# Kernel tuning notes

Hardware: AMD Instinct MI355X
Metric: run time of the kernel (lower is better)

The kernel has to match this reference:

```python
import jax, jax.numpy as jnp
import numpy as np

DIM = 1024
NUM_HEADS = 16
HEAD_DIM = DIM // NUM_HEADS
SCALE = HEAD_DIM ** -0.5


def setup_inputs() -> dict:
    key = jax.random.key(0)
    ks = jax.random.split(key, 5)
    x = jax.random.normal(ks[0], (8, 1024, DIM), dtype=jnp.float32)
    # nn.Linear default init ~ U(-1/sqrt(fan_in), 1/sqrt(fan_in)); use scaled normals
    w_qkv = jax.random.normal(ks[1], (DIM, 3 * DIM), dtype=jnp.float32) * (DIM ** -0.5)
    b_qkv = jax.random.normal(ks[2], (3 * DIM,), dtype=jnp.float32) * 0.02
    w_proj = jax.random.normal(ks[3], (DIM, DIM), dtype=jnp.float32) * (DIM ** -0.5)
    b_proj = jax.random.normal(ks[4], (DIM,), dtype=jnp.float32) * 0.02
    return {"x": x, "w_qkv": w_qkv, "b_qkv": b_qkv, "w_proj": w_proj, "b_proj": b_proj}


def reference(x, w_qkv, b_qkv, w_proj, b_proj):
    B, N, D = x.shape
    qkv = x @ w_qkv + b_qkv                       # [B, N, 3D]
    qkv = qkv.reshape(B, N, 3, NUM_HEADS, HEAD_DIM)
    qkv = jnp.transpose(qkv, (2, 0, 3, 1, 4))     # [3, B, H, N, hd]
    q, k, v = qkv[0], qkv[1], qkv[2]
    attn = jnp.einsum('bhqd,bhkd->bhqk', q, k) * SCALE
    attn = jax.nn.softmax(attn, axis=-1)
    out = jnp.einsum('bhqk,bhkd->bhqd', attn, v)  # [B, H, N, hd]
    out = jnp.transpose(out, (0, 2, 1, 3)).reshape(B, N, D)
    out = out @ w_proj + b_proj
    return out
```

## Files before the change

kernel.cpp:

```cpp
#include <hip/hip_runtime.h>
#include <stdint.h>


typedef short bf16x8 __attribute__((ext_vector_type(8)));
typedef float f32x4 __attribute__((ext_vector_type(4)));

__device__ __forceinline__ short f32_bf16(float f) {
  uint32_t u = __builtin_bit_cast(uint32_t, f);
  u += 0x7FFFu + ((u >> 16) & 1u);
  return (short)(u >> 16);
}

__device__ __forceinline__ float bf16_f32(short s) {
  uint32_t u = ((uint32_t)(uint16_t)s) << 16;
  return __builtin_bit_cast(float, u);
}

__device__ __forceinline__ void gload_lds16(const void* g, void* l) {
  __builtin_amdgcn_global_load_lds(
      (const __attribute__((address_space(1))) uint32_t*)g,
      (__attribute__((address_space(3))) uint32_t*)l, 16, 0, 0);
}

__global__ __launch_bounds__(256) void convert_x_kernel(
    const float* __restrict__ x, short* __restrict__ xb) {
  int i = blockIdx.x * 256 + threadIdx.x;
  const float4 f0 = ((const float4*)x)[i * 2];
  const float4 f1 = ((const float4*)x)[i * 2 + 1];
  bf16x8 o;
  o[0] = f32_bf16(f0.x); o[1] = f32_bf16(f0.y);
  o[2] = f32_bf16(f0.z); o[3] = f32_bf16(f0.w);
  o[4] = f32_bf16(f1.x); o[5] = f32_bf16(f1.y);
  o[6] = f32_bf16(f1.z); o[7] = f32_bf16(f1.w);
  ((bf16x8*)xb)[i] = o;
}

__global__ __launch_bounds__(256) void transpose_w_kernel(
    const float* __restrict__ w, short* __restrict__ wt, int N) {
  __shared__ float tile[64][65];
  const int n0 = blockIdx.x * 64, k0 = blockIdx.y * 64;
  const int tr = threadIdx.x >> 6, tc = threadIdx.x & 63;
#pragma unroll
  for (int i = 0; i < 16; ++i) {
    int k = tr + i * 4;
    tile[k][tc] = w[(size_t)(k0 + k) * N + n0 + tc];
  }
  __syncthreads();
#pragma unroll
  for (int i = 0; i < 16; ++i) {
    int a = tr + i * 4;
    wt[(size_t)(n0 + a) * 1024 + k0 + tc] = f32_bf16(tile[tc][a]);
  }
}

__global__ __launch_bounds__(256, 2) void gemm_qkv_kernel(
    const short* __restrict__ A, const short* __restrict__ Bt,
    const float* __restrict__ bias, short* __restrict__ Qb,
    short* __restrict__ Kb, short* __restrict__ Vt) {
  __shared__ short Asm[128 * 64];
  __shared__ short Bsm[128 * 64];
  const int tid = threadIdx.x;
  const int lane = tid & 63;
  const int w = tid >> 6;
  const int wr = w >> 1, wc = w & 1;
  const int c = lane & 15, g = lane >> 4;

  const int NT = 24;
  const int tm = blockIdx.x / NT, tn = blockIdx.x % NT;
  const int m0 = tm * 128, n0 = tn * 128;

  f32x4 acc[4][4] = {};

  for (int k0 = 0; k0 < 1024; k0 += 64) {
#pragma unroll
    for (int i = 0; i < 4; ++i) {
      int ch = (w * 4 + i) * 64 + lane;
      int r = ch >> 3, c8 = ch & 7;
      gload_lds16(A + (size_t)(m0 + r) * 1024 + k0 + c8 * 8, &Asm[ch * 8]);
      gload_lds16(Bt + (size_t)(n0 + r) * 1024 + k0 + c8 * 8, &Bsm[ch * 8]);
    }
    asm volatile("s_waitcnt vmcnt(0)" ::: "memory");
    __syncthreads();
#pragma unroll
    for (int kk = 0; kk < 2; ++kk) {
      bf16x8 a[4], b[4];
#pragma unroll
      for (int m = 0; m < 4; ++m)
        a[m] = *(const bf16x8*)&Asm[(wr * 64 + m * 16 + c) * 64 + kk * 32 + 8 * g];
#pragma unroll
      for (int n = 0; n < 4; ++n)
        b[n] = *(const bf16x8*)&Bsm[(wc * 64 + n * 16 + c) * 64 + kk * 32 + 8 * g];
#pragma unroll
      for (int m = 0; m < 4; ++m)
#pragma unroll
        for (int n = 0; n < 4; ++n)
          acc[m][n] = __builtin_amdgcn_mfma_f32_16x16x32_bf16(a[m], b[n], acc[m][n], 0, 0, 0);
    }
    __syncthreads();
  }

#pragma unroll
  for (int m = 0; m < 4; ++m) {
    const int i_base = m0 + wr * 64 + m * 16 + 4 * g;
#pragma unroll
    for (int n = 0; n < 4; ++n) {
      const int j = n0 + wc * 64 + n * 16 + c;
      const float bj = bias[j];
      const int three = j >> 10, rem = j & 1023, h = rem >> 6, d = rem & 63;
#pragma unroll
      for (int r = 0; r < 4; ++r) {
        const int i = i_base + r;
        const int bb = i >> 10, nn = i & 1023;
        const int bh = bb * 16 + h;
        const short bv = f32_bf16(acc[m][n][r] + bj);
        if (three == 0)
          Qb[(size_t)(bh * 1024 + nn) * 64 + d] = bv;
        else if (three == 1)
          Kb[(size_t)(bh * 1024 + nn) * 64 + d] = bv;
        else
          Vt[(size_t)(bh * 64 + d) * 1024 + nn] = bv;
      }
    }
  }
}

__global__ __launch_bounds__(256, 2) void attn_kernel(
    const short* __restrict__ Qb, const short* __restrict__ Kb,
    const short* __restrict__ Vt, short* __restrict__ Ao) {
  __shared__ short Kf[8 * 64 * 8];
  __shared__ short Vf[8 * 64 * 8];
  __shared__ short Pl[4][16 * 72];

  const int tid = threadIdx.x, lane = tid & 63, w = tid >> 6;
  const int c = lane & 15, g = lane >> 4;
  const int bh = blockIdx.x >> 3, qb = blockIdx.x & 7;
  const int bb = bh >> 4, h = bh & 15;
  const int q0 = qb * 128 + w * 32;

  bf16x8 qf[2][2];
#pragma unroll
  for (int m = 0; m < 2; ++m)
#pragma unroll
    for (int ks = 0; ks < 2; ++ks)
      qf[m][ks] = *(const bf16x8*)(Qb + (size_t)(bh * 1024 + q0 + m * 16 + c) * 64 + ks * 32 + 8 * g);

  f32x4 o[2][4] = {};
  float mrun[2][4], lrun[2][4];
#pragma unroll
  for (int m = 0; m < 2; ++m)
#pragma unroll
    for (int r = 0; r < 4; ++r) { mrun[m][r] = -1e30f; lrun[m][r] = 0.f; }

  const int row_r = tid >> 2;
  const int seg = tid & 3;

  for (int t = 0; t < 16; ++t) {
    const int kv0 = t * 64;
    {
      const short* src = Kb + (size_t)(bh * 1024 + kv0 + row_r) * 64 + seg * 16;
      bf16x8 v0 = *(const bf16x8*)(src);
      bf16x8 v1 = *(const bf16x8*)(src + 8);
      const int kt = row_r >> 4;
#pragma unroll
      for (int hh = 0; hh < 2; ++hh) {
        const int d0 = seg * 16 + hh * 8;
        const int ks = d0 >> 5;
        const int slot = (row_r & 15) + 16 * ((d0 & 31) >> 3);
        *(bf16x8*)&Kf[((kt * 2 + ks) * 64 + slot) * 8] = hh ? v1 : v0;
      }
      const short* vsrc = Vt + (size_t)(bh * 64 + row_r) * 1024 + kv0 + seg * 16;
      bf16x8 u0 = *(const bf16x8*)(vsrc);
      bf16x8 u1 = *(const bf16x8*)(vsrc + 8);
      const int dt = row_r >> 4;
#pragma unroll
      for (int hh = 0; hh < 2; ++hh) {
        const int k0l = seg * 16 + hh * 8;
        const int kk = k0l >> 5;
        const int slot = (row_r & 15) + 16 * ((k0l & 31) >> 3);
        *(bf16x8*)&Vf[((dt * 2 + kk) * 64 + slot) * 8] = hh ? u1 : u0;
      }
    }
    __syncthreads();

#pragma unroll
    for (int m = 0; m < 2; ++m) {
      f32x4 s[4];
#pragma unroll
      for (int kt = 0; kt < 4; ++kt) {
        f32x4 sa = {};
#pragma unroll
        for (int ks = 0; ks < 2; ++ks) {
          bf16x8 kb = *(const bf16x8*)&Kf[((kt * 2 + ks) * 64 + lane) * 8];
          sa = __builtin_amdgcn_mfma_f32_16x16x32_bf16(qf[m][ks], kb, sa, 0, 0, 0);
        }
        s[kt] = sa;
      }
#pragma unroll
      for (int kt = 0; kt < 4; ++kt)
#pragma unroll
        for (int r = 0; r < 4; ++r) s[kt][r] *= 0.125f;

      float tmax[4], alpha[4], rsum[4];
#pragma unroll
      for (int r = 0; r < 4; ++r) {
        float v = fmaxf(fmaxf(s[0][r], s[1][r]), fmaxf(s[2][r], s[3][r]));
#pragma unroll
        for (int msk = 1; msk < 16; msk <<= 1) v = fmaxf(v, __shfl_xor(v, msk));
        float mnew = fmaxf(mrun[m][r], v);
        alpha[r] = __expf(mrun[m][r] - mnew);
        mrun[m][r] = mnew;
        rsum[r] = 0.f;
      }
#pragma unroll
      for (int dt = 0; dt < 4; ++dt)
#pragma unroll
        for (int r = 0; r < 4; ++r) o[m][dt][r] *= alpha[r];

#pragma unroll
      for (int kt = 0; kt < 4; ++kt)
#pragma unroll
        for (int r = 0; r < 4; ++r) {
          float p = __expf(s[kt][r] - mrun[m][r]);
          rsum[r] += p;
          Pl[w][(4 * g + r) * 72 + kt * 16 + c] = f32_bf16(p);
        }
#pragma unroll
      for (int r = 0; r < 4; ++r) {
        float v = rsum[r];
#pragma unroll
        for (int msk = 1; msk < 16; msk <<= 1) v += __shfl_xor(v, msk);
        lrun[m][r] = lrun[m][r] * alpha[r] + v;
      }

#pragma unroll
      for (int kk = 0; kk < 2; ++kk) {
        bf16x8 pa = *(const bf16x8*)&Pl[w][c * 72 + kk * 32 + 8 * g];
#pragma unroll
        for (int dt = 0; dt < 4; ++dt) {
          bf16x8 vb = *(const bf16x8*)&Vf[((dt * 2 + kk) * 64 + lane) * 8];
          o[m][dt] = __builtin_amdgcn_mfma_f32_16x16x32_bf16(pa, vb, o[m][dt], 0, 0, 0);
        }
      }
    }
    __syncthreads();
  }

#pragma unroll
  for (int m = 0; m < 2; ++m)
#pragma unroll
    for (int dt = 0; dt < 4; ++dt)
#pragma unroll
      for (int r = 0; r < 4; ++r) {
        const int n = q0 + m * 16 + 4 * g + r;
        const float v = o[m][dt][r] / lrun[m][r];
        Ao[(size_t)(bb * 1024 + n) * 1024 + h * 64 + dt * 16 + c] = f32_bf16(v);
      }
}

__global__ __launch_bounds__(256, 2) void gemm_proj_kernel(
    const short* __restrict__ A, const short* __restrict__ Bt,
    const float* __restrict__ bias, float* __restrict__ out) {
  __shared__ short Asm[128 * 64];
  __shared__ short Bsm[128 * 64];
  const int tid = threadIdx.x;
  const int lane = tid & 63;
  const int w = tid >> 6;
  const int wr = w >> 1, wc = w & 1;
  const int c = lane & 15, g = lane >> 4;

  const int NT = 8;
  const int tm = blockIdx.x / NT, tn = blockIdx.x % NT;
  const int m0 = tm * 128, n0 = tn * 128;

  f32x4 acc[4][4] = {};

  for (int k0 = 0; k0 < 1024; k0 += 64) {
#pragma unroll
    for (int i = 0; i < 4; ++i) {
      int ch = (w * 4 + i) * 64 + lane;
      int r = ch >> 3, c8 = ch & 7;
      gload_lds16(A + (size_t)(m0 + r) * 1024 + k0 + c8 * 8, &Asm[ch * 8]);
      gload_lds16(Bt + (size_t)(n0 + r) * 1024 + k0 + c8 * 8, &Bsm[ch * 8]);
    }
    asm volatile("s_waitcnt vmcnt(0)" ::: "memory");
    __syncthreads();
#pragma unroll
    for (int kk = 0; kk < 2; ++kk) {
      bf16x8 a[4], b[4];
#pragma unroll
      for (int m = 0; m < 4; ++m)
        a[m] = *(const bf16x8*)&Asm[(wr * 64 + m * 16 + c) * 64 + kk * 32 + 8 * g];
#pragma unroll
      for (int n = 0; n < 4; ++n)
        b[n] = *(const bf16x8*)&Bsm[(wc * 64 + n * 16 + c) * 64 + kk * 32 + 8 * g];
#pragma unroll
      for (int m = 0; m < 4; ++m)
#pragma unroll
        for (int n = 0; n < 4; ++n)
          acc[m][n] = __builtin_amdgcn_mfma_f32_16x16x32_bf16(a[m], b[n], acc[m][n], 0, 0, 0);
    }
    __syncthreads();
  }

#pragma unroll
  for (int m = 0; m < 4; ++m) {
    const int i_base = m0 + wr * 64 + m * 16 + 4 * g;
#pragma unroll
    for (int n = 0; n < 4; ++n) {
      const int j = n0 + wc * 64 + n * 16 + c;
      const float bj = bias[j];
#pragma unroll
      for (int r = 0; r < 4; ++r)
        out[(size_t)(i_base + r) * 1024 + j] = acc[m][n][r] + bj;
    }
  }
}

extern "C" void kernel_launch(void* const* d_in, const int* in_sizes, int n_in,
                              void* d_out, int out_size, void* d_ws, size_t ws_size,
                              hipStream_t stream) {
  const float* x = (const float*)d_in[0];
  const float* w_qkv = (const float*)d_in[1];
  const float* b_qkv = (const float*)d_in[2];
  const float* w_proj = (const float*)d_in[3];
  const float* b_proj = (const float*)d_in[4];
  float* out = (float*)d_out;

  char* ws = (char*)d_ws;
  const size_t XB_OFF = 0;
  const size_t WQKVT_OFF = 16777216;
  const size_t WPROJT_OFF = WQKVT_OFF + 6291456;
  const size_t Q_OFF = WPROJT_OFF + 2097152;
  const size_t K_OFF = Q_OFF + 16777216;
  const size_t VT_OFF = K_OFF + 16777216;
  short* xb = (short*)(ws + XB_OFF);
  short* wqkvT = (short*)(ws + WQKVT_OFF);
  short* wprojT = (short*)(ws + WPROJT_OFF);
  short* Qb = (short*)(ws + Q_OFF);
  short* Kb = (short*)(ws + K_OFF);
  short* Vt = (short*)(ws + VT_OFF);
  short* attn_o = xb;

  convert_x_kernel<<<dim3(4096), dim3(256), 0, stream>>>(x, xb);
  transpose_w_kernel<<<dim3(48, 16), dim3(256), 0, stream>>>(w_qkv, wqkvT, 3072);
  transpose_w_kernel<<<dim3(16, 16), dim3(256), 0, stream>>>(w_proj, wprojT, 1024);
  gemm_qkv_kernel<<<dim3(64 * 24), dim3(256), 0, stream>>>(xb, wqkvT, b_qkv, Qb, Kb, Vt);
  attn_kernel<<<dim3(1024), dim3(256), 0, stream>>>(Qb, Kb, Vt, attn_o);
  gemm_proj_kernel<<<dim3(64 * 8), dim3(256), 0, stream>>>(attn_o, wprojT, b_proj, out);
}
```

Measured before the change: 325.0 us.

## Restructure attention softmax with exp2, lazy rescale, transposed MFMA and register prefetch

```diff
diff --git a/kernel.cpp b/kernel.cpp
--- a/kernel.cpp
+++ b/kernel.cpp
@@ -4,6 +4,7 @@
 
 typedef short bf16x8 __attribute__((ext_vector_type(8)));
 typedef float f32x4 __attribute__((ext_vector_type(4)));
+typedef uint32_t u32x2 __attribute__((ext_vector_type(2)));
 
 __device__ __forceinline__ short f32_bf16(float f) {
   uint32_t u = __builtin_bit_cast(uint32_t, f);
@@ -11,9 +12,14 @@
   return (short)(u >> 16);
 }
 
-__device__ __forceinline__ float bf16_f32(short s) {
-  uint32_t u = ((uint32_t)(uint16_t)s) << 16;
-  return __builtin_bit_cast(float, u);
+__device__ __forceinline__ float exp2_fast(float x) {
+  float r; asm("v_exp_f32 %0, %1" : "=v"(r) : "v"(x)); return r;
+}
+
+__device__ __forceinline__ uint32_t cvt_pk_bf16(float lo, float hi) {
+  uint32_t r;
+  asm("v_cvt_pk_bf16_f32 %0, %1, %2" : "=v"(r) : "v"(lo), "v"(hi));
+  return r;
 }
 
 __device__ __forceinline__ void gload_lds16(const void* g, void* l) {
@@ -107,12 +113,13 @@
       const int j = n0 + wc * 64 + n * 16 + c;
       const float bj = bias[j];
       const int three = j >> 10, rem = j & 1023, h = rem >> 6, d = rem & 63;
+      const float sc = (three == 1) ? 0.18033688f : 1.0f;
 #pragma unroll
       for (int r = 0; r < 4; ++r) {
         const int i = i_base + r;
         const int bb = i >> 10, nn = i & 1023;
         const int bh = bb * 16 + h;
-        const short bv = f32_bf16(acc[m][n][r] + bj);
+        const short bv = f32_bf16((acc[m][n][r] + bj) * sc);
         if (three == 0)
           Qb[(size_t)(bh * 1024 + nn) * 64 + d] = bv;
         else if (three == 1)
@@ -127,9 +134,10 @@
 __global__ __launch_bounds__(256, 2) void attn_kernel(
     const short* __restrict__ Qb, const short* __restrict__ Kb,
     const short* __restrict__ Vt, short* __restrict__ Ao) {
-  __shared__ short Kf[8 * 64 * 8];
-  __shared__ short Vf[8 * 64 * 8];
-  __shared__ short Pl[4][16 * 72];
+  __shared__ __align__(16) char smem[25600];
+  short* Kf = (short*)smem;
+  short* Vf = (short*)(smem + 8192);
+  short* Pl = (short*)(smem + 16384);
 
   const int tid = threadIdx.x, lane = tid & 63, w = tid >> 6;
   const int c = lane & 15, g = lane >> 4;
@@ -145,43 +153,27 @@
       qf[m][ks] = *(const bf16x8*)(Qb + (size_t)(bh * 1024 + q0 + m * 16 + c) * 64 + ks * 32 + 8 * g);
 
   f32x4 o[2][4] = {};
-  float mrun[2][4], lrun[2][4];
-#pragma unroll
-  for (int m = 0; m < 2; ++m)
-#pragma unroll
-    for (int r = 0; r < 4; ++r) { mrun[m][r] = -1e30f; lrun[m][r] = 0.f; }
-
-  const int row_r = tid >> 2;
-  const int seg = tid & 3;
-
-  for (int t = 0; t < 16; ++t) {
-    const int kv0 = t * 64;
-    {
-      const short* src = Kb + (size_t)(bh * 1024 + kv0 + row_r) * 64 + seg * 16;
-      bf16x8 v0 = *(const bf16x8*)(src);
-      bf16x8 v1 = *(const bf16x8*)(src + 8);
-      const int kt = row_r >> 4;
-#pragma unroll
-      for (int hh = 0; hh < 2; ++hh) {
-        const int d0 = seg * 16 + hh * 8;
-        const int ks = d0 >> 5;
-        const int slot = (row_r & 15) + 16 * ((d0 & 31) >> 3);
-        *(bf16x8*)&Kf[((kt * 2 + ks) * 64 + slot) * 8] = hh ? v1 : v0;
-      }
-      const short* vsrc = Vt + (size_t)(bh * 64 + row_r) * 1024 + kv0 + seg * 16;
-      bf16x8 u0 = *(const bf16x8*)(vsrc);
-      bf16x8 u1 = *(const bf16x8*)(vsrc + 8);
-      const int dt = row_r >> 4;
-#pragma unroll
-      for (int hh = 0; hh < 2; ++hh) {
-        const int k0l = seg * 16 + hh * 8;
-        const int kk = k0l >> 5;
-        const int slot = (row_r & 15) + 16 * ((k0l & 31) >> 3);
-        *(bf16x8*)&Vf[((dt * 2 + kk) * 64 + slot) * 8] = hh ? u1 : u0;
-      }
-    }
-    __syncthreads();
-
+  float mrun[2] = {-3.0e38f, -3.0e38f};
+  float lrun[2] = {0.f, 0.f};
+
+  const int row_r = tid >> 2, seg = tid & 3;
+  const short* kp = Kb + (size_t)(bh * 1024 + row_r) * 64 + seg * 16;
+  const short* vp = Vt + (size_t)(bh * 64 + row_r) * 1024 + seg * 16;
+  short *kdst0, *kdst1, *vdst0, *vdst1;
+  {
+    const int d0a = seg * 16, d0b = seg * 16 + 8;
+    const int pa = (row_r >> 4) * 2 + (d0a >> 5);
+    const int pb = (row_r >> 4) * 2 + (d0b >> 5);
+    const int sa = (row_r & 15) + 16 * ((d0a & 31) >> 3);
+    const int sb = (row_r & 15) + 16 * ((d0b & 31) >> 3);
+    kdst0 = &Kf[(pa * 64 + sa) * 8]; kdst1 = &Kf[(pb * 64 + sb) * 8];
+    vdst0 = &Vf[(pa * 64 + sa) * 8]; vdst1 = &Vf[(pb * 64 + sb) * 8];
+  }
+
+  uint32_t* plw = (uint32_t*)(Pl + w * 1152);
+  const short* plr = Pl + w * 1152;
+
+  auto compute = [&]() {
 #pragma unroll
     for (int m = 0; m < 2; ++m) {
       f32x4 s[4];
@@ -191,70 +183,106 @@
 #pragma unroll
         for (int ks = 0; ks < 2; ++ks) {
           bf16x8 kb = *(const bf16x8*)&Kf[((kt * 2 + ks) * 64 + lane) * 8];
-          sa = __builtin_amdgcn_mfma_f32_16x16x32_bf16(qf[m][ks], kb, sa, 0, 0, 0);
+          sa = __builtin_amdgcn_mfma_f32_16x16x32_bf16(kb, qf[m][ks], sa, 0, 0, 0);
         }
         s[kt] = sa;
       }
+      float vmax = s[0][0];
 #pragma unroll
       for (int kt = 0; kt < 4; ++kt)
 #pragma unroll
-        for (int r = 0; r < 4; ++r) s[kt][r] *= 0.125f;
-
-      float tmax[4], alpha[4], rsum[4];
-#pragma unroll
-      for (int r = 0; r < 4; ++r) {
-        float v = fmaxf(fmaxf(s[0][r], s[1][r]), fmaxf(s[2][r], s[3][r]));
-#pragma unroll
-        for (int msk = 1; msk < 16; msk <<= 1) v = fmaxf(v, __shfl_xor(v, msk));
-        float mnew = fmaxf(mrun[m][r], v);
-        alpha[r] = __expf(mrun[m][r] - mnew);
-        mrun[m][r] = mnew;
-        rsum[r] = 0.f;
-      }
-#pragma unroll
-      for (int dt = 0; dt < 4; ++dt)
-#pragma unroll
-        for (int r = 0; r < 4; ++r) o[m][dt][r] *= alpha[r];
-
-#pragma unroll
-      for (int kt = 0; kt < 4; ++kt)
-#pragma unroll
-        for (int r = 0; r < 4; ++r) {
-          float p = __expf(s[kt][r] - mrun[m][r]);
-          rsum[r] += p;
-          Pl[w][(4 * g + r) * 72 + kt * 16 + c] = f32_bf16(p);
-        }
-#pragma unroll
-      for (int r = 0; r < 4; ++r) {
-        float v = rsum[r];
-#pragma unroll
-        for (int msk = 1; msk < 16; msk <<= 1) v += __shfl_xor(v, msk);
-        lrun[m][r] = lrun[m][r] * alpha[r] + v;
-      }
-
+        for (int r = 0; r < 4; ++r) vmax = fmaxf(vmax, s[kt][r]);
+      vmax = fmaxf(vmax, __shfl_xor(vmax, 16));
+      vmax = fmaxf(vmax, __shfl_xor(vmax, 32));
+      if (!__all(vmax <= mrun[m] + 8.0f)) {
+        float mnew = fmaxf(mrun[m], vmax);
+        float al = exp2_fast(mrun[m] - mnew);
+        lrun[m] *= al;
+#pragma unroll
+        for (int dt = 0; dt < 4; ++dt) o[m][dt] *= al;
+        mrun[m] = mnew;
+      }
+      float rs = 0.f;
+#pragma unroll
+      for (int kt = 0; kt < 4; ++kt) {
+        float p0 = exp2_fast(s[kt][0] - mrun[m]);
+        float p1 = exp2_fast(s[kt][1] - mrun[m]);
+        float p2 = exp2_fast(s[kt][2] - mrun[m]);
+        float p3 = exp2_fast(s[kt][3] - mrun[m]);
+        rs += (p0 + p1) + (p2 + p3);
+        u32x2 pk;
+        pk[0] = cvt_pk_bf16(p0, p1);
+        pk[1] = cvt_pk_bf16(p2, p3);
+        *(u32x2*)&plw[c * 36 + kt * 8 + 2 * g] = pk;
+      }
+      rs += __shfl_xor(rs, 16);
+      rs += __shfl_xor(rs, 32);
+      lrun[m] += rs;
 #pragma unroll
       for (int kk = 0; kk < 2; ++kk) {
-        bf16x8 pa = *(const bf16x8*)&Pl[w][c * 72 + kk * 32 + 8 * g];
+        bf16x8 pb = *(const bf16x8*)(plr + c * 72 + kk * 32 + 8 * g);
 #pragma unroll
         for (int dt = 0; dt < 4; ++dt) {
           bf16x8 vb = *(const bf16x8*)&Vf[((dt * 2 + kk) * 64 + lane) * 8];
-          o[m][dt] = __builtin_amdgcn_mfma_f32_16x16x32_bf16(pa, vb, o[m][dt], 0, 0, 0);
+          o[m][dt] = __builtin_amdgcn_mfma_f32_16x16x32_bf16(vb, pb, o[m][dt], 0, 0, 0);
         }
       }
     }
-    __syncthreads();
-  }
-
-#pragma unroll
-  for (int m = 0; m < 2; ++m)
+  };
+
+  bf16x8 ka0, ka1, va0, va1, kc0, kc1, vc0, vc1;
+  ka0 = *(const bf16x8*)(kp);     ka1 = *(const bf16x8*)(kp + 8);
+  va0 = *(const bf16x8*)(vp);     va1 = *(const bf16x8*)(vp + 8);
+
+  for (int t = 0; t < 16; t += 2) {
+    __syncthreads();
+    *(bf16x8*)kdst0 = ka0; *(bf16x8*)kdst1 = ka1;
+    *(bf16x8*)vdst0 = va0; *(bf16x8*)vdst1 = va1;
+    {
+      const short* kpt = kp + (size_t)(t + 1) * 4096;
+      const short* vpt = vp + (t + 1) * 64;
+      kc0 = *(const bf16x8*)(kpt); kc1 = *(const bf16x8*)(kpt + 8);
+      vc0 = *(const bf16x8*)(vpt); vc1 = *(const bf16x8*)(vpt + 8);
+    }
+    __syncthreads();
+    compute();
+    __syncthreads();
+    *(bf16x8*)kdst0 = kc0; *(bf16x8*)kdst1 = kc1;
+    *(bf16x8*)vdst0 = vc0; *(bf16x8*)vdst1 = vc1;
+    if (t + 2 < 16) {
+      const short* kpt = kp + (size_t)(t + 2) * 4096;
+      const short* vpt = vp + (t + 2) * 64;
+      ka0 = *(const bf16x8*)(kpt); ka1 = *(const bf16x8*)(kpt + 8);
+      va0 = *(const bf16x8*)(vpt); va1 = *(const bf16x8*)(vpt + 8);
+    }
+    __syncthreads();
+    compute();
+  }
+
+  __syncthreads();
+  float* Osc = (float*)smem + w * (16 * 68);
+  const int qrow = lane >> 2, dseg = (lane & 3) << 4;
+#pragma unroll
+  for (int m = 0; m < 2; ++m) {
+    const float inv = 1.0f / lrun[m];
 #pragma unroll
     for (int dt = 0; dt < 4; ++dt)
 #pragma unroll
-      for (int r = 0; r < 4; ++r) {
-        const int n = q0 + m * 16 + 4 * g + r;
-        const float v = o[m][dt][r] / lrun[m][r];
-        Ao[(size_t)(bb * 1024 + n) * 1024 + h * 64 + dt * 16 + c] = f32_bf16(v);
-      }
+      for (int r = 0; r < 4; ++r)
+        Osc[c * 68 + dt * 16 + 4 * g + r] = o[m][dt][r] * inv;
+#pragma unroll
+    for (int j = 0; j < 2; ++j) {
+      f32x4 a0 = *(f32x4*)&Osc[qrow * 68 + dseg + j * 8];
+      f32x4 a1 = *(f32x4*)&Osc[qrow * 68 + dseg + j * 8 + 4];
+      bf16x8 ob;
+      ob[0] = f32_bf16(a0[0]); ob[1] = f32_bf16(a0[1]);
+      ob[2] = f32_bf16(a0[2]); ob[3] = f32_bf16(a0[3]);
+      ob[4] = f32_bf16(a1[0]); ob[5] = f32_bf16(a1[1]);
+      ob[6] = f32_bf16(a1[2]); ob[7] = f32_bf16(a1[3]);
+      *(bf16x8*)(Ao + (size_t)(bb * 1024 + q0 + m * 16 + qrow) * 1024 + h * 64 + dseg + j * 8) = ob;
+    }
+    __syncthreads();
+  }
 }
 
 __global__ __launch_bounds__(256, 2) void gemm_proj_kernel(
```

Measured after the change: 273.9 us. -15.7%, faster.
